# Kernel optimization log

Measured on AMD Instinct MI355X. Metric: run time of the kernel, lower is better.

The kernel has to match this reference:

```python
import jax, jax.numpy as jnp
import numpy as np

jax.config.update("jax_enable_x64", True)  # faithful int64 LIF state, as in the torch module

NUM_INPUTS = 700
NUM_HIDDEN = 4096
NUM_OUTPUT = 20
N_STEPS = 1000
ALPHA_SHIFT = 4   # synaptic-current decay shift
BETA_SHIFT = 3    # membrane decay shift
THRESHOLD = 1
BW1 = 64
BW2 = 64


def _sat(x, bw):
    # Quantize.saturate + to_int: clamp to signed bw-bit range, cast to int64.
    lo = -(2 ** (bw - 1))
    hi = 2 ** (bw - 1) - 1
    if jnp.issubdtype(x.dtype, jnp.floating):
        # values here are far below 2**63, so the float clip/cast is exact
        return jnp.clip(x, float(lo), float(hi)).astype(jnp.int64)
    return jnp.clip(x, lo, hi)


def _decay(v, shift):
    # LIF.exp_decay: v - (v >> shift) with arithmetic right shift on int64
    return v - (v >> shift)


def setup_inputs() -> dict:
    key = jax.random.key(0)
    k1, k2, k3, k4 = jax.random.split(key, 4)
    input_spikes = jax.random.randint(k1, (N_STEPS, NUM_INPUTS), 0, 2, dtype=jnp.int64)
    w1 = jax.random.randint(k2, (NUM_HIDDEN, NUM_INPUTS), -8, 8, dtype=jnp.int64)
    v1 = jax.random.randint(k3, (NUM_HIDDEN, NUM_HIDDEN), -8, 8, dtype=jnp.int64)
    w2 = jax.random.randint(k4, (NUM_OUTPUT, NUM_HIDDEN), -8, 8, dtype=jnp.int64)
    return {"input_spikes": input_spikes, "w1": w1, "v1": v1, "w2": w2}


def reference(input_spikes, w1, v1, w2):
    w1f = w1.astype(jnp.float32)
    v1f = v1.astype(jnp.float32)
    w2f = w2.astype(jnp.float32)
    # feed-forward input currents for all timesteps at once: [T, H]
    in_all = _sat(jnp.einsum("hi,ti->th", w1f, input_spikes.astype(jnp.float32)), BW1)

    H = w1.shape[0]
    O = w2.shape[0]
    z = lambda n: jnp.zeros((n,), dtype=jnp.int64)
    # state: hidden spikes, hidden mem, hidden syn, readout mem, readout syn
    init = (z(H), z(H), z(H), z(O), z(O))

    def step(state, in_cur):
        h_out, h_mem, h_syn, r_mem, r_syn = state
        # recurrent feedback current from PREVIOUS step's hidden spikes
        fb = _sat(jnp.einsum("hk,k->h", v1f, h_out.astype(jnp.float32)), BW1)
        syn_curr = _sat(in_cur + fb, BW1)
        # hidden LIF: reset (by previous spike) -> threshold -> decay/integrate
        h_mem = jnp.where(h_out == 1, 0, h_mem)
        new_out = (h_mem - THRESHOLD > 0).astype(jnp.int64)
        new_mem = _decay(h_mem, BETA_SHIFT) + h_syn
        new_syn = _decay(h_syn, ALPHA_SHIFT) + syn_curr
        # readout LIF (no reset); records updated membrane
        ro_cur = _sat(jnp.einsum("oh,h->o", w2f, new_out.astype(jnp.float32)), BW2)
        new_rmem = _decay(r_mem, BETA_SHIFT) + r_syn
        new_rsyn = _decay(r_syn, ALPHA_SHIFT) + ro_cur
        return (new_out, new_mem, new_syn, new_rmem, new_rsyn), new_rmem

    _, rec = jax.lax.scan(step, init, in_all)  # rec: [T, O]
    return rec.T  # torch.stack(ro_mem_rec, dim=1) -> [num_output, n_steps]
```

## Files before the change

kernel.cpp:

```cpp
#include <hip/hip_runtime.h>

#define T_STEPS 1000
#define N_IN    700
#define N_HID   4096
#define N_OUT   20
#define NBLK    256
#define NPB     16

typedef unsigned int u32x4 __attribute__((ext_vector_type(4)));
typedef unsigned int u32x2 __attribute__((ext_vector_type(2)));

__device__ __forceinline__ unsigned load_rec4(const unsigned* p) {
    unsigned r;
    asm volatile("global_load_dword %0, %1, off sc0 sc1\n\t"
                 "s_waitcnt vmcnt(0)"
                 : "=v"(r) : "v"(p) : "memory");
    return r;
}
__device__ __forceinline__ void store_rec4(unsigned* p, unsigned v) {
    asm volatile("global_store_dword %0, %1, off sc0 sc1"
                 :: "v"(p), "v"(v) : "memory");
}

__global__ __launch_bounds__(256) void k_transpose_i8(
    const int* __restrict__ in, signed char* __restrict__ out,
    int R, int C, int out_stride)
{
    __shared__ signed char tile[32][33];
    const int cx = blockIdx.x * 32;
    const int ry = blockIdx.y * 32;
    const int tx = threadIdx.x;
    const int ty = threadIdx.y;
#pragma unroll
    for (int r = 0; r < 4; ++r) {
        int row = ry + ty + r * 8;
        int col = cx + tx;
        if (row < R && col < C)
            tile[ty + r * 8][tx] = (signed char)in[(size_t)row * C + col];
    }
    __syncthreads();
#pragma unroll
    for (int r = 0; r < 4; ++r) {
        int c   = cx + ty + r * 8;
        int row = ry + tx;
        if (c < C && row < R)
            out[(size_t)c * out_stride + row] = tile[tx][ty + r * 8];
    }
}

__global__ __launch_bounds__(256) void k_prep_v1n(
    const int* __restrict__ in, unsigned char* __restrict__ out)
{
    __shared__ unsigned char tile[16][64];
    const int k0 = blockIdx.x * 64;
    const int b  = blockIdx.y;
    const int t  = threadIdx.x;
    const int kk = t & 63;
#pragma unroll
    for (int r = 0; r < 4; ++r) {
        int hl = (t >> 6) + r * 4;
        tile[hl][kk] = (unsigned char)(in[(size_t)(b * NPB + hl) * N_HID + k0 + kk] + 8);
    }
    __syncthreads();
    if (t < 64) {
        unsigned w0 = 0, w1 = 0;
#pragma unroll
        for (int j = 0; j < 8; ++j) w0 |= (unsigned)tile[j][t] << (4 * j);
#pragma unroll
        for (int j = 0; j < 8; ++j) w1 |= (unsigned)tile[8 + j][t] << (4 * j);
        u32x2 v = {w0, w1};
        *(u32x2*)(out + ((size_t)b << 15) + ((size_t)(k0 + t) << 3)) = v;
    }
}

__global__ __launch_bounds__(256) void k_inall(
    const signed char* __restrict__ w1t,
    const int* __restrict__ spk,
    short* __restrict__ in_all2)
{
    __shared__ int s_spk[16][N_IN];
    const int t0 = blockIdx.y * 16;
    const int tcnt = min(16, T_STEPS - t0);
    const int tid = threadIdx.x;
    for (int b = 0; b < tcnt; ++b)
        for (int i = tid; i < N_IN; i += 256)
            s_spk[b][i] = spk[(size_t)(t0 + b) * N_IN + i];
    __syncthreads();
    const int h = blockIdx.x * 256 + tid;
    int acc[16];
#pragma unroll
    for (int b = 0; b < 16; ++b) acc[b] = 0;
    for (int i = 0; i < N_IN; ++i) {
        int w = (int)w1t[(size_t)i * N_HID + h];
#pragma unroll
        for (int b = 0; b < 16; ++b) acc[b] += w * s_spk[b][i];
    }
    const size_t base = (size_t)(h >> 4) * (T_STEPS * NPB) + (h & 15);
    for (int b = 0; b < tcnt; ++b)
        in_all2[base + (size_t)(t0 + b) * NPB] = (short)acc[b];
}

__global__ __launch_bounds__(64) void k_main(
    const short* __restrict__ in_all2,
    const u32x2* __restrict__ v1n,
    unsigned* __restrict__ pub)
{
    const int lane = threadIdx.x;
    const int bid  = blockIdx.x;
    const int j    = lane & 15;

    __shared__ u32x2 s_w[N_HID];
    __shared__ u32x4 s_rec[2][64];

    {
        const u32x2* src = v1n + ((size_t)bid << 12);
        for (int r = lane; r < N_HID; r += 64) s_w[r] = src[r];
    }
    asm volatile("s_waitcnt vmcnt(0) lgkmcnt(0)" ::: "memory");

    if (lane == 0) store_rec4(pub + bid, 0x10000u);

    int mm = 0, synv = 0, out_t = 0;
    const short* in_base = in_all2 + (size_t)bid * (T_STEPS * NPB) + j;
    const u32x2* wl = s_w + (lane << 6);
    const unsigned NM = 0x000F000Fu;

    for (int t = 0; t < T_STEPS; ++t) {
        const int cur = t & 1;
        asm volatile("s_waitcnt vmcnt(0)" ::: "memory");
        __builtin_amdgcn_sched_barrier(0);

        int mem_t = (mm - (mm >> 3)) + synv;
        int mnext = out_t ? 0 : mem_t;
        int out_n = (mnext - 1 > 0) ? 1 : 0;
        unsigned om = (unsigned)__ballot(out_n) & 0xFFFFu;
        if (lane == 0) store_rec4(pub + (size_t)(t + 1) * NBLK + bid, 0x10000u | om);
        mm = mnext; out_t = out_n;

        int in_cur = (int)in_base[t * NPB];

        __builtin_amdgcn_global_load_lds(
            (const void*)(pub + (size_t)t * NBLK + (lane << 2)),
            (void*)&s_rec[cur ^ 1][0], 16, 0,  17);

        unsigned mlo = 0, mhi = 0;
        if (t > 0) {
            u32x4 q = s_rec[cur][lane];
            if (((q.x & q.y & q.z & q.w) & 0x10000u) == 0u) {
                const unsigned* rp = pub + (size_t)(t - 1) * NBLK + (lane << 2);
                while (!(q.x & 0x10000u)) { __builtin_amdgcn_s_sleep(1); q.x = load_rec4(rp + 0); }
                while (!(q.y & 0x10000u)) { __builtin_amdgcn_s_sleep(1); q.y = load_rec4(rp + 1); }
                while (!(q.z & 0x10000u)) { __builtin_amdgcn_s_sleep(1); q.z = load_rec4(rp + 2); }
                while (!(q.w & 0x10000u)) { __builtin_amdgcn_s_sleep(1); q.w = load_rec4(rp + 3); }
            }
            mlo = (q.x & 0xFFFFu) | ((q.y & 0xFFFFu) << 16);
            mhi = (q.z & 0xFFFFu) | ((q.w & 0xFFFFu) << 16);
        }
        unsigned long long m = ((unsigned long long)mhi << 32) | mlo;
        int myc = __popcll(m);

        unsigned a0=0,a1=0,a2=0,a3=0,a4=0,a5=0,a6=0,a7=0;
#define ACC(v) do { \
            a0 += (v).x & NM;         a1 += ((v).x >> 4)  & NM; \
            a2 += ((v).x >> 8) & NM;  a3 += ((v).x >> 12) & NM; \
            a4 += (v).y & NM;         a5 += ((v).y >> 4)  & NM; \
            a6 += ((v).y >> 8) & NM;  a7 += ((v).y >> 12) & NM; } while (0)
        u32x2 p0={0,0}, p1={0,0}, p2={0,0}, p3={0,0};
        int b;
        if (m) { b = __builtin_ctzll(m); m &= m - 1; p0 = wl[b]; }
        if (m) { b = __builtin_ctzll(m); m &= m - 1; p1 = wl[b]; }
        if (m) { b = __builtin_ctzll(m); m &= m - 1; p2 = wl[b]; }
        if (m) { b = __builtin_ctzll(m); m &= m - 1; p3 = wl[b]; }
        while (m) {
            u32x2 n0={0,0}, n1={0,0}, n2={0,0}, n3={0,0};
            if (m) { b = __builtin_ctzll(m); m &= m - 1; n0 = wl[b]; }
            if (m) { b = __builtin_ctzll(m); m &= m - 1; n1 = wl[b]; }
            if (m) { b = __builtin_ctzll(m); m &= m - 1; n2 = wl[b]; }
            if (m) { b = __builtin_ctzll(m); m &= m - 1; n3 = wl[b]; }
            ACC(p0); ACC(p1); ACC(p2); ACC(p3);
            p0 = n0; p1 = n1; p2 = n2; p3 = n3;
        }
        ACC(p0); ACC(p1); ACC(p2); ACC(p3);
#undef ACC

#pragma unroll
        for (int s = 1; s <= 32; s <<= 1) {
            a0 += __shfl_xor(a0, s); a1 += __shfl_xor(a1, s);
            a2 += __shfl_xor(a2, s); a3 += __shfl_xor(a3, s);
            a4 += __shfl_xor(a4, s); a5 += __shfl_xor(a5, s);
            a6 += __shfl_xor(a6, s); a7 += __shfl_xor(a7, s);
            myc += __shfl_xor(myc, s);
        }

        unsigned g0 = (j & 1) ? a1 : a0, g1 = (j & 1) ? a3 : a2;
        unsigned g2 = (j & 1) ? a5 : a4, g3 = (j & 1) ? a7 : a6;
        unsigned h0 = (j & 2) ? g1 : g0, h1 = (j & 2) ? g3 : g2;
        unsigned sel = (j & 8) ? h1 : h0;
        int field = (j & 4) ? (int)(sel >> 16) : (int)(sel & 0xFFFFu);
        int fb = field - 8 * myc;

        synv = (synv - (synv >> 4)) + in_cur + fb;
    }
}

__global__ __launch_bounds__(256) void k_rocur(
    const int* __restrict__ w2,
    const unsigned* __restrict__ pub,
    int* __restrict__ ro)
{
    const int t = blockIdx.x;
    const int tid = threadIdx.x;
    __shared__ unsigned short s_list[N_HID];
    __shared__ int s_red[32][8];
    __shared__ int s_n;
    if (tid < 64) {
        const unsigned* rp = pub + (size_t)t * NBLK + (tid << 2);
        unsigned long long m =
            (unsigned long long)((rp[0] & 0xFFFFu) | ((rp[1] & 0xFFFFu) << 16)) |
            ((unsigned long long)((rp[2] & 0xFFFFu) | ((rp[3] & 0xFFFFu) << 16)) << 32);
        int cnt = __popcll(m);
        int inc = cnt;
#pragma unroll
        for (int d = 1; d < 64; d <<= 1) {
            int v = __shfl_up(inc, d);
            if (tid >= d) inc += v;
        }
        int p = inc - cnt;
        while (m) {
            s_list[p++] = (unsigned short)((tid << 6) | __builtin_ctzll(m));
            m &= m - 1;
        }
        if (tid == 63) s_n = inc;
    }
    __syncthreads();
    const int n = s_n;
    const int o = tid >> 3;
    const int r = tid & 7;
    if (o < N_OUT) {
        int acc = 0;
        for (int jj = r; jj < n; jj += 8) acc += w2[(size_t)o * N_HID + s_list[jj]];
        s_red[o][r] = acc;
    }
    __syncthreads();
    if (tid < N_OUT) {
        int acc = 0;
#pragma unroll
        for (int q = 0; q < 8; ++q) acc += s_red[tid][q];
        ro[(size_t)t * N_OUT + tid] = acc;
    }
}

#define CH 250
__global__ __launch_bounds__(256) void k_scan(const int* __restrict__ ro,
                                              int* __restrict__ out)
{
    __shared__ int s_ro[CH * N_OUT];
    __shared__ int s_out[CH * N_OUT];
    const int tid = threadIdx.x;
    int rm = 0, rs = 0;
    for (int c = 0; c < T_STEPS / CH; ++c) {
        for (int i = tid; i < CH * N_OUT; i += 256)
            s_ro[i] = ro[c * CH * N_OUT + i];
        __syncthreads();
        if (tid < N_OUT) {
            for (int jj = 0; jj < CH; ++jj) {
                rm = (rm - (rm >> 3)) + rs;
                rs = (rs - (rs >> 4)) + s_ro[jj * N_OUT + tid];
                s_out[jj * N_OUT + tid] = rm;
            }
        }
        __syncthreads();
        for (int i = tid; i < CH * N_OUT; i += 256) {
            int o = i / CH, jj = i - o * CH;
            out[o * T_STEPS + c * CH + jj] = s_out[jj * N_OUT + o];
        }
        __syncthreads();
    }
}

extern "C" void kernel_launch(void* const* d_in, const int* in_sizes, int n_in,
                              void* d_out, int out_size, void* d_ws, size_t ws_size,
                              hipStream_t stream)
{
    const int* spk = (const int*)d_in[0];
    const int* w1  = (const int*)d_in[1];
    const int* v1  = (const int*)d_in[2];
    const int* w2  = (const int*)d_in[3];
    int* out = (int*)d_out;

    char* ws = (char*)d_ws;
    constexpr size_t SZ_PUB    = (size_t)(T_STEPS + 1) * NBLK * 4;
    constexpr size_t OFF_PUB   = 0;
    constexpr size_t OFF_INALL = OFF_PUB + SZ_PUB;
    constexpr size_t OFF_V1N   = OFF_INALL + 8192000;
    constexpr size_t OFF_W1T   = OFF_V1N + 8388608;
    constexpr size_t OFF_RO    = OFF_W1T + 2867200;

    unsigned*       pub    = (unsigned*)(ws + OFF_PUB);
    short*          in_all = (short*)(ws + OFF_INALL);
    unsigned char*  v1n    = (unsigned char*)(ws + OFF_V1N);
    signed char*    w1t    = (signed char*)(ws + OFF_W1T);
    int*            ro     = (int*)(ws + OFF_RO);

    hipMemsetAsync(pub, 0, SZ_PUB, stream);

    dim3 tb(32, 8);
    k_prep_v1n<<<dim3(64, 256), 256, 0, stream>>>(v1, v1n);
    k_transpose_i8<<<dim3(22, 128), tb, 0, stream>>>(w1, w1t, N_HID, N_IN, N_HID);
    k_inall<<<dim3(16, 63), 256, 0, stream>>>(w1t, spk, in_all);

    k_main<<<dim3(NBLK), dim3(64), 0, stream>>>(in_all, (const u32x2*)v1n, pub);

    k_rocur<<<dim3(T_STEPS), 256, 0, stream>>>(w2, pub, ro);
    k_scan<<<1, 256, 0, stream>>>(ro, out);
}
```

Before: 1.733 ms.

## Use 8-bit SWAR accumulation, wave-uniform 16-wide batches and a recursive-halving reduction

The inner recurrent gather now accumulates weight nibbles in 8-bit lanes over fixed batches of 16 spikes before widening to 16-bit, which roughly halves the mask/add work per gathered weight. The loop is made wave-uniform with __any and a zero padding row in LDS, so inactive lanes gather zeros instead of diverging. The cross-lane reduction is restructured as a recursive-halving butterfly that exchanges fewer registers per shuffle stage. In exchange, each lane always does 16 gathers per iteration even when it has few spikes, and the 8-bit fields rely on at most 16 additions of 4-bit values to avoid overflow.

```diff
diff --git a/kernel.cpp b/kernel.cpp
--- a/kernel.cpp
+++ b/kernel.cpp
@@ -109,12 +109,13 @@
     const int bid  = blockIdx.x;
     const int j    = lane & 15;
 
-    __shared__ u32x2 s_w[N_HID];
+    __shared__ u32x2 s_w[N_HID + 1];
     __shared__ u32x4 s_rec[2][64];
 
     {
         const u32x2* src = v1n + ((size_t)bid << 12);
         for (int r = lane; r < N_HID; r += 64) s_w[r] = src[r];
+        if (lane == 0) { u32x2 z = {0u, 0u}; s_w[N_HID] = z; }
     }
     asm volatile("s_waitcnt vmcnt(0) lgkmcnt(0)" ::: "memory");
 
@@ -123,7 +124,9 @@
     int mm = 0, synv = 0, out_t = 0;
     const short* in_base = in_all2 + (size_t)bid * (T_STEPS * NPB) + j;
     const u32x2* wl = s_w + (lane << 6);
-    const unsigned NM = 0x000F000Fu;
+    const int bz = N_HID - (lane << 6);
+    const unsigned M4 = 0x0F0F0F0Fu, M8 = 0x00FF00FFu;
+    const int j0 = j & 1, j1 = j & 2, j3 = j & 8;
 
     for (int t = 0; t < T_STEPS; ++t) {
         const int cur = t & 1;
@@ -160,43 +163,37 @@
         int myc = __popcll(m);
 
         unsigned a0=0,a1=0,a2=0,a3=0,a4=0,a5=0,a6=0,a7=0;
-#define ACC(v) do { \
-            a0 += (v).x & NM;         a1 += ((v).x >> 4)  & NM; \
-            a2 += ((v).x >> 8) & NM;  a3 += ((v).x >> 12) & NM; \
-            a4 += (v).y & NM;         a5 += ((v).y >> 4)  & NM; \
-            a6 += ((v).y >> 8) & NM;  a7 += ((v).y >> 12) & NM; } while (0)
-        u32x2 p0={0,0}, p1={0,0}, p2={0,0}, p3={0,0};
-        int b;
-        if (m) { b = __builtin_ctzll(m); m &= m - 1; p0 = wl[b]; }
-        if (m) { b = __builtin_ctzll(m); m &= m - 1; p1 = wl[b]; }
-        if (m) { b = __builtin_ctzll(m); m &= m - 1; p2 = wl[b]; }
-        if (m) { b = __builtin_ctzll(m); m &= m - 1; p3 = wl[b]; }
-        while (m) {
-            u32x2 n0={0,0}, n1={0,0}, n2={0,0}, n3={0,0};
-            if (m) { b = __builtin_ctzll(m); m &= m - 1; n0 = wl[b]; }
-            if (m) { b = __builtin_ctzll(m); m &= m - 1; n1 = wl[b]; }
-            if (m) { b = __builtin_ctzll(m); m &= m - 1; n2 = wl[b]; }
-            if (m) { b = __builtin_ctzll(m); m &= m - 1; n3 = wl[b]; }
-            ACC(p0); ACC(p1); ACC(p2); ACC(p3);
-            p0 = n0; p1 = n1; p2 = n2; p3 = n3;
-        }
-        ACC(p0); ACC(p1); ACC(p2); ACC(p3);
-#undef ACC
-
-#pragma unroll
-        for (int s = 1; s <= 32; s <<= 1) {
-            a0 += __shfl_xor(a0, s); a1 += __shfl_xor(a1, s);
-            a2 += __shfl_xor(a2, s); a3 += __shfl_xor(a3, s);
-            a4 += __shfl_xor(a4, s); a5 += __shfl_xor(a5, s);
-            a6 += __shfl_xor(a6, s); a7 += __shfl_xor(a7, s);
-            myc += __shfl_xor(myc, s);
-        }
-
-        unsigned g0 = (j & 1) ? a1 : a0, g1 = (j & 1) ? a3 : a2;
-        unsigned g2 = (j & 1) ? a5 : a4, g3 = (j & 1) ? a7 : a6;
-        unsigned h0 = (j & 2) ? g1 : g0, h1 = (j & 2) ? g3 : g2;
-        unsigned sel = (j & 8) ? h1 : h0;
-        int field = (j & 4) ? (int)(sel >> 16) : (int)(sel & 0xFFFFu);
+        while (__any((int)(m != 0ull))) {
+            unsigned be0=0, bo0=0, be1=0, bo1=0;
+#pragma unroll
+            for (int u = 0; u < 16; ++u) {
+                int b = m ? (int)__builtin_ctzll(m) : bz;
+                m &= m - 1;
+                u32x2 w = wl[b];
+                be0 += w.x & M4;  bo0 += (w.x >> 4) & M4;
+                be1 += w.y & M4;  bo1 += (w.y >> 4) & M4;
+            }
+            a0 += be0 & M8;  a1 += (be0 >> 8) & M8;
+            a2 += bo0 & M8;  a3 += (bo0 >> 8) & M8;
+            a4 += be1 & M8;  a5 += (be1 >> 8) & M8;
+            a6 += bo1 & M8;  a7 += (bo1 >> 8) & M8;
+        }
+
+        unsigned e0 = (j0 ? a2 : a0) + __shfl_xor(j0 ? a0 : a2, 1);
+        unsigned e1 = (j0 ? a3 : a1) + __shfl_xor(j0 ? a1 : a3, 1);
+        unsigned e2 = (j0 ? a6 : a4) + __shfl_xor(j0 ? a4 : a6, 1);
+        unsigned e3 = (j0 ? a7 : a5) + __shfl_xor(j0 ? a5 : a7, 1);
+        unsigned f0 = (j1 ? e1 : e0) + __shfl_xor(j1 ? e0 : e1, 2);
+        unsigned f1 = (j1 ? e3 : e2) + __shfl_xor(j1 ? e2 : e3, 2);
+        unsigned g  = (j3 ? f1 : f0) + __shfl_xor(j3 ? f0 : f1, 8);
+        g += __shfl_xor(g, 4);
+        g += __shfl_xor(g, 16);
+        g += __shfl_xor(g, 32);
+        myc += __shfl_xor(myc, 1);  myc += __shfl_xor(myc, 2);
+        myc += __shfl_xor(myc, 4);  myc += __shfl_xor(myc, 8);
+        myc += __shfl_xor(myc, 16); myc += __shfl_xor(myc, 32);
+
+        int field = (int)((g >> ((j & 4) << 2)) & 0xFFFFu);
         int fb = field - 8 * myc;
 
         synv = (synv - (synv >> 4)) + in_cur + fb;
```

New measurement: 1.952 ms. 12.6% more time.
